# Kernel tuning notes

Measured on AMD Instinct MI355X. Metric: run time of the kernel, lower is better.

The kernel has to match this reference:

```python
import jax, jax.numpy as jnp
import numpy as np

B, L, E, S = 4, 1024, 256, 32  # batch, seq_len, e_dim, local window half-size
NEG = -1e30  # stands in for excluding out-of-range positions from softmax


def setup_inputs() -> dict:
    key = jax.random.key(0)
    ks = jax.random.split(key, 8)
    sc = 1.0 / np.sqrt(E)
    return {
        "q": jax.random.normal(ks[0], (B, L, E), jnp.float32),
        "Wq": jax.random.normal(ks[1], (E, E), jnp.float32) * sc,
        "bq": jax.random.normal(ks[2], (E,), jnp.float32) * sc,
        "Wk": jax.random.normal(ks[3], (E, E), jnp.float32) * sc,
        "bk": jax.random.normal(ks[4], (E,), jnp.float32) * sc,
        "Wv": jax.random.normal(ks[5], (E, E), jnp.float32) * sc,
        "bv": jax.random.normal(ks[6], (E,), jnp.float32) * sc,
        "pos_bias": jax.random.normal(ks[7], (2 * S + 1, E), jnp.float32),
    }


def reference(q, Wq, bq, Wk, bk, Wv, bv, pos_bias):
    # Linear projections (nn.Linear: x @ W.T + b)
    Q = q @ Wq.T + bq
    K = q @ Wk.T + bk
    V = q @ Wv.T + bv

    W = 2 * S + 1
    rel = jnp.arange(-S, S + 1)                      # [W] relative offsets
    idx = jnp.arange(L)[:, None] + rel[None, :]       # [L, W] absolute positions
    valid = (idx >= 0) & (idx < L)                    # in-sequence window entries
    idxc = jnp.clip(idx, 0, L - 1)
    strict = jnp.abs(rel) < S                         # |j-i| < s mask (zeroes K at edges)

    # Gather windows: [B, L, W, E]
    K_win = K[:, idxc] + pos_bias[rel + S][None, None, :, :]
    K_masked = jnp.where(strict[None, None, :, None], K_win, 0.0)
    # Out-of-range positions excluded from softmax entirely (logit -> -inf)
    logits = jnp.where(valid[None, :, :, None], Q[:, :, None, :] * K_masked, NEG)
    weights = jax.nn.softmax(logits, axis=2)          # per-channel softmax over window

    V_win = jnp.where(valid[None, :, :, None], V[:, idxc], 0.0)
    ctx = jnp.sum(weights * V_win, axis=2)            # [B, L, E]

    sig = jax.nn.sigmoid(Q)
    # sigmoid applied inside the loop and again at the end -> squared
    return sig * sig * ctx
```

## Files before the change

### kernel.cpp

```cpp
#include <hip/hip_runtime.h>
#include <hip/hip_bf16.h>

#define B_ 4
#define L_ 1024
#define E_ 256
#define S_ 32

typedef __bf16 bf16x8 __attribute__((ext_vector_type(8)));
typedef float f32x4 __attribute__((ext_vector_type(4)));

__device__ __forceinline__ __bf16 bf_from_bits(unsigned short u) {
    __bf16 b;
    __builtin_memcpy(&b, &u, 2);
    return b;
}

__device__ __forceinline__ void load8split(const float* __restrict__ p,
                                           bf16x8& h, bf16x8& l) {
    const float4 x0 = *(const float4*)p;
    const float4 x1 = *(const float4*)(p + 4);
    const float xs[8] = {x0.x, x0.y, x0.z, x0.w, x1.x, x1.y, x1.z, x1.w};
#pragma unroll
    for (int j = 0; j < 8; ++j) {
        const unsigned hb = __float_as_uint(xs[j]) & 0xFFFF0000u;
        h[j] = bf_from_bits((unsigned short)(hb >> 16));
        l[j] = (__bf16)(xs[j] - __uint_as_float(hb));
    }
}

__global__ __launch_bounds__(256, 1) void qkv_gemm2(
    const float* __restrict__ A,
    const float* __restrict__ Wq, const float* __restrict__ bq,
    const float* __restrict__ Wk, const float* __restrict__ bk,
    const float* __restrict__ Wv, const float* __restrict__ bv,
    float* __restrict__ Qo, float* __restrict__ Ko, float* __restrict__ Vo)
{
    const float* Wm;
    const float* bm;
    float* Om;
    const int z = blockIdx.z;
    if (z == 0)      { Wm = Wq; bm = bq; Om = Qo; }
    else if (z == 1) { Wm = Wk; bm = bk; Om = Ko; }
    else             { Wm = Wv; bm = bv; Om = Vo; }

    const int wave = threadIdx.x >> 6;
    const int lane = threadIdx.x & 63;
    const int rsel = lane & 15;
    const int koff = (lane >> 4) * 8;

    const int m0 = blockIdx.x * 32;
    const int nb = wave * 64;

    const float* pa0 = A + (size_t)(m0 + rsel) * 256 + koff;
    const float* pa1 = pa0 + (size_t)16 * 256;
    const float* pw0 = Wm + (size_t)(nb + 0  + rsel) * 256 + koff;
    const float* pw1 = Wm + (size_t)(nb + 16 + rsel) * 256 + koff;
    const float* pw2 = Wm + (size_t)(nb + 32 + rsel) * 256 + koff;
    const float* pw3 = Wm + (size_t)(nb + 48 + rsel) * 256 + koff;

    f32x4 acc[2][4];
#pragma unroll
    for (int mt = 0; mt < 2; ++mt)
#pragma unroll
        for (int nt = 0; nt < 4; ++nt)
            acc[mt][nt] = (f32x4){0.f, 0.f, 0.f, 0.f};

#pragma unroll
    for (int k0 = 0; k0 < 256; k0 += 32) {
        bf16x8 ah[2], al[2], bh[4], bl[4];
        load8split(pa0 + k0, ah[0], al[0]);
        load8split(pa1 + k0, ah[1], al[1]);
        load8split(pw0 + k0, bh[0], bl[0]);
        load8split(pw1 + k0, bh[1], bl[1]);
        load8split(pw2 + k0, bh[2], bl[2]);
        load8split(pw3 + k0, bh[3], bl[3]);
#pragma unroll
        for (int mt = 0; mt < 2; ++mt)
#pragma unroll
            for (int nt = 0; nt < 4; ++nt) {
                acc[mt][nt] = __builtin_amdgcn_mfma_f32_16x16x32_bf16(
                    ah[mt], bh[nt], acc[mt][nt], 0, 0, 0);
                acc[mt][nt] = __builtin_amdgcn_mfma_f32_16x16x32_bf16(
                    ah[mt], bl[nt], acc[mt][nt], 0, 0, 0);
                acc[mt][nt] = __builtin_amdgcn_mfma_f32_16x16x32_bf16(
                    al[mt], bh[nt], acc[mt][nt], 0, 0, 0);
            }
    }

#pragma unroll
    for (int mt = 0; mt < 2; ++mt) {
        const int mrow = m0 + mt * 16 + (lane >> 4) * 4;
#pragma unroll
        for (int nt = 0; nt < 4; ++nt) {
            const int n = nb + nt * 16 + rsel;
            const float bias = bm[n];
#pragma unroll
            for (int r = 0; r < 4; ++r)
                Om[(size_t)(mrow + r) * 256 + n] = acc[mt][nt][r] + bias;
        }
    }
}

#define TI2 32
#define CH2 64
#define HB2 96
#define PS2 68

__global__ __launch_bounds__(256) void aft_stage2b(
    const float* __restrict__ Q, const float* __restrict__ K,
    const float* __restrict__ V, const float* __restrict__ pb,
    float* __restrict__ out)
{
    __shared__ float Kw[HB2][PS2];
    __shared__ float Vw[HB2][PS2];
    __shared__ float Pw[2 * S_ + 1][PS2];

    const int tid = threadIdx.x;
    const int b  = blockIdx.y;
    const int i0 = blockIdx.x * TI2;
    const int c0 = blockIdx.z * CH2;

    const float* Kb = K + (size_t)b * L_ * E_;
    const float* Vb = V + (size_t)b * L_ * E_;

    for (int idx = tid; idx < HB2 * 16; idx += 256) {
        const int r  = idx >> 4;
        const int cq = (idx & 15) * 4;
        int j = i0 - S_ + r;
        j = j < 0 ? 0 : (j > L_ - 1 ? L_ - 1 : j);
        const size_t g = (size_t)j * E_ + c0 + cq;
        *(float4*)&Kw[r][cq] = *(const float4*)(Kb + g);
        *(float4*)&Vw[r][cq] = *(const float4*)(Vb + g);
    }
    for (int idx = tid; idx < (2 * S_ + 1) * 16; idx += 256) {
        const int r  = idx >> 4;
        const int cq = (idx & 15) * 4;
        *(float4*)&Pw[r][cq] = *(const float4*)(pb + (size_t)r * E_ + c0 + cq);
    }
    __syncthreads();

    const int cq = (tid & 15) * 4;
    const int is = tid >> 4;

#pragma unroll
    for (int rep = 0; rep < 2; ++rep) {
        const int rr = is + rep * 16;
        const int i  = i0 + rr;

        const float4 qv = *(const float4*)(Q + ((size_t)b * L_ + i) * E_ + c0 + cq);

        float den0 = 0.f, den1 = 0.f, den2 = 0.f, den3 = 0.f;
        float num0 = 0.f, num1 = 0.f, num2 = 0.f, num3 = 0.f;

        const int jlo = (i - S_ < 0) ? 0 : (i - S_);
        const int jhi = (i + S_ > L_ - 1) ? (L_ - 1) : (i + S_);

        for (int j = jlo; j <= jhi; ++j) {
            const int r = j - (i0 - S_);
            const int w = j - i + S_;
            const float4 vv = *(const float4*)&Vw[r][cq];

            float kx = 0.f, ky = 0.f, kz = 0.f, kw = 0.f;
            if (w != 0 && w != 2 * S_) {
                const float4 kk = *(const float4*)&Kw[r][cq];
                const float4 pp = *(const float4*)&Pw[w][cq];
                kx = kk.x + pp.x;
                ky = kk.y + pp.y;
                kz = kk.z + pp.z;
                kw = kk.w + pp.w;
            }
            const float e0 = __expf(qv.x * kx);
            const float e1 = __expf(qv.y * ky);
            const float e2 = __expf(qv.z * kz);
            const float e3 = __expf(qv.w * kw);
            den0 += e0; den1 += e1; den2 += e2; den3 += e3;
            num0 += e0 * vv.x; num1 += e1 * vv.y;
            num2 += e2 * vv.z; num3 += e3 * vv.w;
        }

        const float s0 = 1.f / (1.f + __expf(-qv.x));
        const float s1 = 1.f / (1.f + __expf(-qv.y));
        const float s2 = 1.f / (1.f + __expf(-qv.z));
        const float s3 = 1.f / (1.f + __expf(-qv.w));

        float4 o;
        o.x = s0 * s0 * num0 / den0;
        o.y = s1 * s1 * num1 / den1;
        o.z = s2 * s2 * num2 / den2;
        o.w = s3 * s3 * num3 / den3;
        *(float4*)(out + ((size_t)b * L_ + i) * E_ + c0 + cq) = o;
    }
}

#define TI 32
#define CG 64
#define RK 96
#define LDP 68

__global__ __launch_bounds__(256) void aft_fused(
    const float* __restrict__ q,
    const float* __restrict__ Wq, const float* __restrict__ bq,
    const float* __restrict__ Wk, const float* __restrict__ bk,
    const float* __restrict__ Wv, const float* __restrict__ bv,
    const float* __restrict__ pb,
    float* __restrict__ out)
{
    __shared__ float Kl[RK][LDP];
    __shared__ float Vl[RK][LDP];
    __shared__ float Ql[TI][LDP];

    const int i0 = blockIdx.x * TI;
    const int b  = blockIdx.y;
    const int c0 = blockIdx.z * CG;

    const int wave = threadIdx.x >> 6;
    const int lane = threadIdx.x & 63;
    const int rsel = lane & 15;
    const int koff = (lane >> 4) * 8;

    const float* qb = q + (size_t)b * L_ * E_;

    for (int job = wave; job < 56; job += 4) {
        int p, rt, ct;
        if (job < 24)      { p = 0; rt = job >> 2;        ct = job & 3; }
        else if (job < 48) { p = 1; rt = (job - 24) >> 2; ct = (job - 24) & 3; }
        else               { p = 2; rt = (job - 48) >> 2; ct = (job - 48) & 3; }

        int jrow = (p == 2) ? (i0 + rt * 16 + rsel)
                            : (i0 - S_ + rt * 16 + rsel);
        int jc = jrow < 0 ? 0 : (jrow > L_ - 1 ? L_ - 1 : jrow);
        const float* pa = qb + (size_t)jc * E_ + koff;

        const float* Wm = (p == 0) ? Wk : (p == 1) ? Wv : Wq;
        const float* bm = (p == 0) ? bk : (p == 1) ? bv : bq;
        const int n = c0 + ct * 16 + rsel;
        const float* pw = Wm + (size_t)n * E_ + koff;

        f32x4 acc = {0.f, 0.f, 0.f, 0.f};
#pragma unroll
        for (int k0 = 0; k0 < 256; k0 += 32) {
            bf16x8 ah, al, bh, bl;
            load8split(pa + k0, ah, al);
            load8split(pw + k0, bh, bl);
            acc = __builtin_amdgcn_mfma_f32_16x16x32_bf16(ah, bh, acc, 0, 0, 0);
            acc = __builtin_amdgcn_mfma_f32_16x16x32_bf16(ah, bl, acc, 0, 0, 0);
            acc = __builtin_amdgcn_mfma_f32_16x16x32_bf16(al, bh, acc, 0, 0, 0);
        }

        const float bias = bm[n];
        const int row0 = rt * 16 + (lane >> 4) * 4;
        const int colc = ct * 16 + rsel;
        float* dst = (p == 0) ? &Kl[0][0] : (p == 1) ? &Vl[0][0] : &Ql[0][0];
#pragma unroll
        for (int r = 0; r < 4; ++r)
            dst[(size_t)(row0 + r) * LDP + colc] = acc[r] + bias;
    }
    __syncthreads();

    const int cq  = threadIdx.x & 15;
    const int is0 = threadIdx.x >> 4;
    const int cL  = cq * 4;
    const int cG  = c0 + cL;
    const float* pbc = pb + cG;

    for (int rr = is0; rr < TI; rr += 16) {
        const int i = i0 + rr;
        const float4 qv = *(const float4*)&Ql[rr][cL];

        float den0 = 0.f, den1 = 0.f, den2 = 0.f, den3 = 0.f;
        float num0 = 0.f, num1 = 0.f, num2 = 0.f, num3 = 0.f;

        const int jlo = (i - S_ < 0) ? 0 : (i - S_);
        const int jhi = (i + S_ > L_ - 1) ? (L_ - 1) : (i + S_);

        for (int j = jlo; j <= jhi; ++j) {
            const int r = j - (i0 - S_);
            const int w = j - i + S_;
            const float4 vv = *(const float4*)&Vl[r][cL];

            float kx = 0.f, ky = 0.f, kz = 0.f, kw = 0.f;
            if (w != 0 && w != 2 * S_) {
                const float4 kk = *(const float4*)&Kl[r][cL];
                const float4 pp = *(const float4*)(pbc + (size_t)w * E_);
                kx = kk.x + pp.x;
                ky = kk.y + pp.y;
                kz = kk.z + pp.z;
                kw = kk.w + pp.w;
            }
            const float e0 = __expf(qv.x * kx);
            const float e1 = __expf(qv.y * ky);
            const float e2 = __expf(qv.z * kz);
            const float e3 = __expf(qv.w * kw);
            den0 += e0; den1 += e1; den2 += e2; den3 += e3;
            num0 += e0 * vv.x; num1 += e1 * vv.y;
            num2 += e2 * vv.z; num3 += e3 * vv.w;
        }

        const float s0 = 1.f / (1.f + __expf(-qv.x));
        const float s1 = 1.f / (1.f + __expf(-qv.y));
        const float s2 = 1.f / (1.f + __expf(-qv.z));
        const float s3 = 1.f / (1.f + __expf(-qv.w));

        float4 o;
        o.x = s0 * s0 * num0 / den0;
        o.y = s1 * s1 * num1 / den1;
        o.z = s2 * s2 * num2 / den2;
        o.w = s3 * s3 * num3 / den3;
        *(float4*)(out + ((size_t)b * L_ + i) * E_ + cG) = o;
    }
}

extern "C" void kernel_launch(void* const* d_in, const int* in_sizes, int n_in,
                              void* d_out, int out_size, void* d_ws, size_t ws_size,
                              hipStream_t stream) {
    const float* q  = (const float*)d_in[0];
    const float* Wq = (const float*)d_in[1];
    const float* bq = (const float*)d_in[2];
    const float* Wk = (const float*)d_in[3];
    const float* bk = (const float*)d_in[4];
    const float* Wv = (const float*)d_in[5];
    const float* bv = (const float*)d_in[6];
    const float* pb = (const float*)d_in[7];

    const size_t needA = (size_t)3 * 4096 * 256 * sizeof(float);

    if (ws_size >= needA) {
        float* Qf = (float*)d_ws;
        float* Kf = Qf + (size_t)4096 * 256;
        float* Vf = Kf + (size_t)4096 * 256;
        qkv_gemm2<<<dim3(128, 1, 3), 256, 0, stream>>>(q, Wq, bq, Wk, bk, Wv, bv,
                                                       Qf, Kf, Vf);
        aft_stage2b<<<dim3(L_ / TI2, B_, E_ / CH2), 256, 0, stream>>>(
            Qf, Kf, Vf, pb, (float*)d_out);
    } else {
        aft_fused<<<dim3(L_ / TI, B_, E_ / CG), 256, 0, stream>>>(
            q, Wq, bq, Wk, bk, Wv, bv, pb, (float*)d_out);
    }
}
```

Baseline: 124.4 us.

## Rewrite local-window softmax stage with 4-row register blocking and exp2

Replaces the stage-2 windowed softmax kernel with one in which each thread handles four consecutive query rows over two channels. Each K/V row read from shared memory is reused across the four rows, and positional-bias values are rotated through registers. Interior blocks skip the bounds masks entirely, and the edge taps whose logit is zero are peeled into explicit prologue and epilogue steps. Exp is computed as exp2 on Q pre-scaled by log2(e). Blocks shrink to 128 threads over 32 channels, which doubles the grid to improve occupancy and load balance, at the cost of more register pressure and larger, more complex code.

```diff
diff --git a/kernel.cpp b/kernel.cpp
--- a/kernel.cpp
+++ b/kernel.cpp
@@ -8,11 +8,27 @@
 
 typedef __bf16 bf16x8 __attribute__((ext_vector_type(8)));
 typedef float f32x4 __attribute__((ext_vector_type(4)));
+typedef float f32x2 __attribute__((ext_vector_type(2)));
 
 __device__ __forceinline__ __bf16 bf_from_bits(unsigned short u) {
     __bf16 b;
     __builtin_memcpy(&b, &u, 2);
     return b;
+}
+
+__device__ __forceinline__ float fexp2(float x) {
+#if __has_builtin(__builtin_amdgcn_exp2f)
+    return __builtin_amdgcn_exp2f(x);
+#else
+    return exp2f(x);
+#endif
+}
+
+__device__ __forceinline__ f32x2 vexp2(f32x2 t) {
+    f32x2 r;
+    r.x = fexp2(t.x);
+    r.y = fexp2(t.y);
+    return r;
 }
 
 __device__ __forceinline__ void load8split(const float* __restrict__ p,
@@ -101,95 +117,280 @@
     }
 }
 
-#define TI2 32
-#define CH2 64
-#define HB2 96
-#define PS2 68
-
-__global__ __launch_bounds__(256) void aft_stage2b(
+#define TI7 32
+#define CH7 32
+#define HR7 96
+#define PS7 36
+
+#define STEP4I(T, PNEW, PH1, PH2, PH3)                                   \
+    {                                                                    \
+        const int rl = rb + (T);                                         \
+        const f32x2 kk = *(const f32x2*)&Kw[rl][c];                      \
+        const f32x2 vv = *(const f32x2*)&Vw[rl][c];                      \
+        PNEW = *(const f32x2*)&Pw[(T)][c];                               \
+        const f32x2 e0 = vexp2(qs0 * (kk + PNEW));                       \
+        const f32x2 e1 = vexp2(qs1 * (kk + PH1));                        \
+        const f32x2 e2 = vexp2(qs2 * (kk + PH2));                        \
+        const f32x2 e3 = vexp2(qs3 * (kk + PH3));                        \
+        d0 += e0; n0 += e0 * vv;                                         \
+        d1 += e1; n1 += e1 * vv;                                         \
+        d2 += e2; n2 += e2 * vv;                                         \
+        d3 += e3; n3 += e3 * vv;                                         \
+    }
+
+#define STEP4E(T, PNEW, PH1, PH2, PH3)                                   \
+    {                                                                    \
+        const int jj = iA - S_ + (T);                                    \
+        const float m = (jj >= 0 && jj <= L_ - 1) ? 1.f : 0.f;           \
+        const int rl = rb + (T);                                         \
+        const f32x2 kk = *(const f32x2*)&Kw[rl][c];                      \
+        const f32x2 vv = *(const f32x2*)&Vw[rl][c];                      \
+        PNEW = *(const f32x2*)&Pw[(T)][c];                               \
+        const f32x2 e0 = m * vexp2(qs0 * (kk + PNEW));                   \
+        const f32x2 e1 = m * vexp2(qs1 * (kk + PH1));                    \
+        const f32x2 e2 = m * vexp2(qs2 * (kk + PH2));                    \
+        const f32x2 e3 = m * vexp2(qs3 * (kk + PH3));                    \
+        d0 += e0; n0 += e0 * vv;                                         \
+        d1 += e1; n1 += e1 * vv;                                         \
+        d2 += e2; n2 += e2 * vv;                                         \
+        d3 += e3; n3 += e3 * vv;                                         \
+    }
+
+__global__ __launch_bounds__(128, 2) void aft_stage2h(
     const float* __restrict__ Q, const float* __restrict__ K,
     const float* __restrict__ V, const float* __restrict__ pb,
     float* __restrict__ out)
 {
-    __shared__ float Kw[HB2][PS2];
-    __shared__ float Vw[HB2][PS2];
-    __shared__ float Pw[2 * S_ + 1][PS2];
+    __shared__ float Kw[HR7][PS7];
+    __shared__ float Vw[HR7][PS7];
+    __shared__ float Pw[2 * S_ + 1][PS7];
 
     const int tid = threadIdx.x;
     const int b  = blockIdx.y;
-    const int i0 = blockIdx.x * TI2;
-    const int c0 = blockIdx.z * CH2;
+    const int i0 = blockIdx.x * TI7;
+    const int c0 = blockIdx.z * CH7;
+
+    const int duo = tid & 15;
+    const int qd  = tid >> 4;
+    const int c   = duo * 2;
+    const int iA  = i0 + qd * 4;
+    const int rb  = qd * 4;
+
+    const float* Qr = Q + ((size_t)b * L_ + iA) * E_ + c0 + c;
+    const f32x2 qv0 = *(const f32x2*)(Qr);
+    const f32x2 qv1 = *(const f32x2*)(Qr + E_);
+    const f32x2 qv2 = *(const f32x2*)(Qr + 2 * E_);
+    const f32x2 qv3 = *(const f32x2*)(Qr + 3 * E_);
 
     const float* Kb = K + (size_t)b * L_ * E_;
     const float* Vb = V + (size_t)b * L_ * E_;
 
-    for (int idx = tid; idx < HB2 * 16; idx += 256) {
-        const int r  = idx >> 4;
-        const int cq = (idx & 15) * 4;
+    for (int idx = tid; idx < HR7 * 8; idx += 128) {
+        const int r = idx >> 3;
+        const int cc = (idx & 7) * 4;
         int j = i0 - S_ + r;
         j = j < 0 ? 0 : (j > L_ - 1 ? L_ - 1 : j);
-        const size_t g = (size_t)j * E_ + c0 + cq;
-        *(float4*)&Kw[r][cq] = *(const float4*)(Kb + g);
-        *(float4*)&Vw[r][cq] = *(const float4*)(Vb + g);
-    }
-    for (int idx = tid; idx < (2 * S_ + 1) * 16; idx += 256) {
-        const int r  = idx >> 4;
-        const int cq = (idx & 15) * 4;
-        *(float4*)&Pw[r][cq] = *(const float4*)(pb + (size_t)r * E_ + c0 + cq);
+        const size_t g = (size_t)j * E_ + c0 + cc;
+        *(float4*)&Kw[r][cc] = *(const float4*)(Kb + g);
+        *(float4*)&Vw[r][cc] = *(const float4*)(Vb + g);
+    }
+    for (int idx = tid; idx < (2 * S_ + 1) * 8; idx += 128) {
+        const int r = idx >> 3;
+        const int cc = (idx & 7) * 4;
+        *(float4*)&Pw[r][cc] = *(const float4*)(pb + (size_t)r * E_ + c0 + cc);
     }
     __syncthreads();
 
-    const int cq = (tid & 15) * 4;
-    const int is = tid >> 4;
-
-#pragma unroll
-    for (int rep = 0; rep < 2; ++rep) {
-        const int rr = is + rep * 16;
-        const int i  = i0 + rr;
-
-        const float4 qv = *(const float4*)(Q + ((size_t)b * L_ + i) * E_ + c0 + cq);
-
-        float den0 = 0.f, den1 = 0.f, den2 = 0.f, den3 = 0.f;
-        float num0 = 0.f, num1 = 0.f, num2 = 0.f, num3 = 0.f;
-
-        const int jlo = (i - S_ < 0) ? 0 : (i - S_);
-        const int jhi = (i + S_ > L_ - 1) ? (L_ - 1) : (i + S_);
-
-        for (int j = jlo; j <= jhi; ++j) {
-            const int r = j - (i0 - S_);
-            const int w = j - i + S_;
-            const float4 vv = *(const float4*)&Vw[r][cq];
-
-            float kx = 0.f, ky = 0.f, kz = 0.f, kw = 0.f;
-            if (w != 0 && w != 2 * S_) {
-                const float4 kk = *(const float4*)&Kw[r][cq];
-                const float4 pp = *(const float4*)&Pw[w][cq];
-                kx = kk.x + pp.x;
-                ky = kk.y + pp.y;
-                kz = kk.z + pp.z;
-                kw = kk.w + pp.w;
-            }
-            const float e0 = __expf(qv.x * kx);
-            const float e1 = __expf(qv.y * ky);
-            const float e2 = __expf(qv.z * kz);
-            const float e3 = __expf(qv.w * kw);
-            den0 += e0; den1 += e1; den2 += e2; den3 += e3;
-            num0 += e0 * vv.x; num1 += e1 * vv.y;
-            num2 += e2 * vv.z; num3 += e3 * vv.w;
-        }
-
-        const float s0 = 1.f / (1.f + __expf(-qv.x));
-        const float s1 = 1.f / (1.f + __expf(-qv.y));
-        const float s2 = 1.f / (1.f + __expf(-qv.z));
-        const float s3 = 1.f / (1.f + __expf(-qv.w));
-
-        float4 o;
-        o.x = s0 * s0 * num0 / den0;
-        o.y = s1 * s1 * num1 / den1;
-        o.z = s2 * s2 * num2 / den2;
-        o.w = s3 * s3 * num3 / den3;
-        *(float4*)(out + ((size_t)b * L_ + i) * E_ + c0 + cq) = o;
-    }
+    const float LOG2E = 1.44269504088896340736f;
+    const f32x2 qs0 = qv0 * LOG2E;
+    const f32x2 qs1 = qv1 * LOG2E;
+    const f32x2 qs2 = qv2 * LOG2E;
+    const f32x2 qs3 = qv3 * LOG2E;
+
+    f32x2 d0 = {0.f, 0.f}, n0 = {0.f, 0.f};
+    f32x2 d1 = {0.f, 0.f}, n1 = {0.f, 0.f};
+    f32x2 d2 = {0.f, 0.f}, n2 = {0.f, 0.f};
+    f32x2 d3 = {0.f, 0.f}, n3 = {0.f, 0.f};
+
+    f32x2 p0, h1, h2, h3;
+
+    const bool interior = (blockIdx.x >= 1) && (blockIdx.x <= (L_ / TI7) - 2);
+
+    if (interior) {
+        {
+            const f32x2 vv = *(const f32x2*)&Vw[rb][c];
+            d0 += 1.f; n0 += vv;
+        }
+        {
+            const f32x2 kk = *(const f32x2*)&Kw[rb + 1][c];
+            const f32x2 vv = *(const f32x2*)&Vw[rb + 1][c];
+            h3 = *(const f32x2*)&Pw[1][c];
+            const f32x2 e0 = vexp2(qs0 * (kk + h3));
+            d0 += e0; n0 += e0 * vv;
+            d1 += 1.f; n1 += vv;
+        }
+        {
+            const f32x2 kk = *(const f32x2*)&Kw[rb + 2][c];
+            const f32x2 vv = *(const f32x2*)&Vw[rb + 2][c];
+            h2 = *(const f32x2*)&Pw[2][c];
+            const f32x2 e0 = vexp2(qs0 * (kk + h2));
+            const f32x2 e1 = vexp2(qs1 * (kk + h3));
+            d0 += e0; n0 += e0 * vv;
+            d1 += e1; n1 += e1 * vv;
+            d2 += 1.f; n2 += vv;
+        }
+        {
+            const f32x2 kk = *(const f32x2*)&Kw[rb + 3][c];
+            const f32x2 vv = *(const f32x2*)&Vw[rb + 3][c];
+            h1 = *(const f32x2*)&Pw[3][c];
+            const f32x2 e0 = vexp2(qs0 * (kk + h1));
+            const f32x2 e1 = vexp2(qs1 * (kk + h2));
+            const f32x2 e2 = vexp2(qs2 * (kk + h3));
+            d0 += e0; n0 += e0 * vv;
+            d1 += e1; n1 += e1 * vv;
+            d2 += e2; n2 += e2 * vv;
+            d3 += 1.f; n3 += vv;
+        }
+#pragma unroll 2
+        for (int t = 4; t <= 60; t += 4) {
+            STEP4I(t + 0, p0, h1, h2, h3)
+            STEP4I(t + 1, h3, p0, h1, h2)
+            STEP4I(t + 2, h2, h3, p0, h1)
+            STEP4I(t + 3, h1, h2, h3, p0)
+        }
+        {
+            const f32x2 kk = *(const f32x2*)&Kw[rb + 64][c];
+            const f32x2 vv = *(const f32x2*)&Vw[rb + 64][c];
+            const f32x2 e1 = vexp2(qs1 * (kk + h1));
+            const f32x2 e2 = vexp2(qs2 * (kk + h2));
+            const f32x2 e3 = vexp2(qs3 * (kk + h3));
+            d0 += 1.f; n0 += vv;
+            d1 += e1; n1 += e1 * vv;
+            d2 += e2; n2 += e2 * vv;
+            d3 += e3; n3 += e3 * vv;
+        }
+        {
+            const f32x2 kk = *(const f32x2*)&Kw[rb + 65][c];
+            const f32x2 vv = *(const f32x2*)&Vw[rb + 65][c];
+            const f32x2 e2 = vexp2(qs2 * (kk + h1));
+            const f32x2 e3 = vexp2(qs3 * (kk + h2));
+            d1 += 1.f; n1 += vv;
+            d2 += e2; n2 += e2 * vv;
+            d3 += e3; n3 += e3 * vv;
+        }
+        {
+            const f32x2 kk = *(const f32x2*)&Kw[rb + 66][c];
+            const f32x2 vv = *(const f32x2*)&Vw[rb + 66][c];
+            const f32x2 e3 = vexp2(qs3 * (kk + h1));
+            d2 += 1.f; n2 += vv;
+            d3 += e3; n3 += e3 * vv;
+        }
+        {
+            const f32x2 vv = *(const f32x2*)&Vw[rb + 67][c];
+            d3 += 1.f; n3 += vv;
+        }
+    } else {
+        {
+            const int jj = iA - S_;
+            const float m = (jj >= 0) ? 1.f : 0.f;
+            const f32x2 vv = *(const f32x2*)&Vw[rb][c];
+            d0 += m; n0 += m * vv;
+        }
+        {
+            const int jj = iA - S_ + 1;
+            const float m = (jj >= 0 && jj <= L_ - 1) ? 1.f : 0.f;
+            const f32x2 kk = *(const f32x2*)&Kw[rb + 1][c];
+            const f32x2 vv = *(const f32x2*)&Vw[rb + 1][c];
+            h3 = *(const f32x2*)&Pw[1][c];
+            const f32x2 e0 = m * vexp2(qs0 * (kk + h3));
+            d0 += e0; n0 += e0 * vv;
+            d1 += m;  n1 += m * vv;
+        }
+        {
+            const int jj = iA - S_ + 2;
+            const float m = (jj >= 0 && jj <= L_ - 1) ? 1.f : 0.f;
+            const f32x2 kk = *(const f32x2*)&Kw[rb + 2][c];
+            const f32x2 vv = *(const f32x2*)&Vw[rb + 2][c];
+            h2 = *(const f32x2*)&Pw[2][c];
+            const f32x2 e0 = m * vexp2(qs0 * (kk + h2));
+            const f32x2 e1 = m * vexp2(qs1 * (kk + h3));
+            d0 += e0; n0 += e0 * vv;
+            d1 += e1; n1 += e1 * vv;
+            d2 += m;  n2 += m * vv;
+        }
+        {
+            const int jj = iA - S_ + 3;
+            const float m = (jj >= 0 && jj <= L_ - 1) ? 1.f : 0.f;
+            const f32x2 kk = *(const f32x2*)&Kw[rb + 3][c];
+            const f32x2 vv = *(const f32x2*)&Vw[rb + 3][c];
+            h1 = *(const f32x2*)&Pw[3][c];
+            const f32x2 e0 = m * vexp2(qs0 * (kk + h1));
+            const f32x2 e1 = m * vexp2(qs1 * (kk + h2));
+            const f32x2 e2 = m * vexp2(qs2 * (kk + h3));
+            d0 += e0; n0 += e0 * vv;
+            d1 += e1; n1 += e1 * vv;
+            d2 += e2; n2 += e2 * vv;
+            d3 += m;  n3 += m * vv;
+        }
+#pragma unroll 2
+        for (int t = 4; t <= 60; t += 4) {
+            STEP4E(t + 0, p0, h1, h2, h3)
+            STEP4E(t + 1, h3, p0, h1, h2)
+            STEP4E(t + 2, h2, h3, p0, h1)
+            STEP4E(t + 3, h1, h2, h3, p0)
+        }
+        {
+            const int jj = iA - S_ + 64;
+            const float m = (jj >= 0 && jj <= L_ - 1) ? 1.f : 0.f;
+            const f32x2 kk = *(const f32x2*)&Kw[rb + 64][c];
+            const f32x2 vv = *(const f32x2*)&Vw[rb + 64][c];
+            const f32x2 e1 = m * vexp2(qs1 * (kk + h1));
+            const f32x2 e2 = m * vexp2(qs2 * (kk + h2));
+            const f32x2 e3 = m * vexp2(qs3 * (kk + h3));
+            d0 += m;  n0 += m * vv;
+            d1 += e1; n1 += e1 * vv;
+            d2 += e2; n2 += e2 * vv;
+            d3 += e3; n3 += e3 * vv;
+        }
+        {
+            const int jj = iA - S_ + 65;
+            const float m = (jj >= 0 && jj <= L_ - 1) ? 1.f : 0.f;
+            const f32x2 kk = *(const f32x2*)&Kw[rb + 65][c];
+            const f32x2 vv = *(const f32x2*)&Vw[rb + 65][c];
+            const f32x2 e2 = m * vexp2(qs2 * (kk + h1));
+            const f32x2 e3 = m * vexp2(qs3 * (kk + h2));
+            d1 += m;  n1 += m * vv;
+            d2 += e2; n2 += e2 * vv;
+            d3 += e3; n3 += e3 * vv;
+        }
+        {
+            const int jj = iA - S_ + 66;
+            const float m = (jj >= 0 && jj <= L_ - 1) ? 1.f : 0.f;
+            const f32x2 kk = *(const f32x2*)&Kw[rb + 66][c];
+            const f32x2 vv = *(const f32x2*)&Vw[rb + 66][c];
+            const f32x2 e3 = m * vexp2(qs3 * (kk + h1));
+            d2 += m;  n2 += m * vv;
+            d3 += e3; n3 += e3 * vv;
+        }
+        {
+            const int jj = iA - S_ + 67;
+            const float m = (jj >= 0 && jj <= L_ - 1) ? 1.f : 0.f;
+            const f32x2 vv = *(const f32x2*)&Vw[rb + 67][c];
+            d3 += m; n3 += m * vv;
+        }
+    }
+
+    f32x2 s0, s1, s2, s3;
+    s0.x = 1.f / (1.f + fexp2(-qs0.x)); s0.y = 1.f / (1.f + fexp2(-qs0.y));
+    s1.x = 1.f / (1.f + fexp2(-qs1.x)); s1.y = 1.f / (1.f + fexp2(-qs1.y));
+    s2.x = 1.f / (1.f + fexp2(-qs2.x)); s2.y = 1.f / (1.f + fexp2(-qs2.y));
+    s3.x = 1.f / (1.f + fexp2(-qs3.x)); s3.y = 1.f / (1.f + fexp2(-qs3.y));
+
+    float* ob = out + ((size_t)b * L_ + iA) * E_ + c0 + c;
+    *(f32x2*)(ob)          = s0 * s0 * n0 / d0;
+    *(f32x2*)(ob + E_)     = s1 * s1 * n1 / d1;
+    *(f32x2*)(ob + 2 * E_) = s2 * s2 * n2 / d2;
+    *(f32x2*)(ob + 3 * E_) = s3 * s3 * n3 / d3;
 }
 
 #define TI 32
@@ -330,7 +531,7 @@
         float* Vf = Kf + (size_t)4096 * 256;
         qkv_gemm2<<<dim3(128, 1, 3), 256, 0, stream>>>(q, Wq, bq, Wk, bk, Wv, bv,
                                                        Qf, Kf, Vf);
-        aft_stage2b<<<dim3(L_ / TI2, B_, E_ / CH2), 256, 0, stream>>>(
+        aft_stage2h<<<dim3(L_ / TI7, B_, E_ / CH7), 128, 0, stream>>>(
             Qf, Kf, Vf, pb, (float*)d_out);
     } else {
         aft_fused<<<dim3(L_ / TI, B_, E_ / CG), 256, 0, stream>>>(
```

After: 112.9 us. 1.1x faster.
